# Optimization experiments

Measured on AMD Instinct MI355X. Metric: run time of the kernel, lower is better.

The kernel has to match this reference:

```python
import jax, jax.numpy as jnp
import numpy as np

N_NODES = 50000
N_EDGES = 800000
NUM_GRAPHS = 256
H = 128          # h_dim
C = H + 1        # CGConv channels = 129
Z = 2 * C + 1    # concat(x_i, x_j, edge_attr) = 259
N_GRAPH_LAYERS = 5
N_FC = 3
OUT_DIM = 1


def setup_inputs() -> dict:
    key = jax.random.key(0)
    ks = jax.random.split(key, 12)
    atoms = jax.random.randint(ks[0], (N_NODES,), 0, 119)
    pos = jax.random.normal(ks[1], (N_NODES, 3), dtype=jnp.float32)
    edge_index = jax.random.randint(ks[2], (2, N_EDGES), 0, N_NODES)
    batch = jnp.sort(jax.random.randint(ks[3], (N_NODES,), 0, NUM_GRAPHS))
    s = 0.05
    emb = jax.random.normal(ks[4], (119, H), dtype=jnp.float32)
    Wf = jax.random.normal(ks[5], (N_GRAPH_LAYERS, Z, C), dtype=jnp.float32) * s
    bf = jnp.zeros((N_GRAPH_LAYERS, C), dtype=jnp.float32)
    Ws = jax.random.normal(ks[6], (N_GRAPH_LAYERS, Z, C), dtype=jnp.float32) * s
    bs = jnp.zeros((N_GRAPH_LAYERS, C), dtype=jnp.float32)
    Wfc = jax.random.normal(ks[7], (N_FC, C, C), dtype=jnp.float32) * s
    bfc = jnp.zeros((N_FC, C), dtype=jnp.float32)
    Wout = jax.random.normal(ks[8], (C, OUT_DIM), dtype=jnp.float32) * s
    bout = jnp.zeros((OUT_DIM,), dtype=jnp.float32)
    return {"atoms": atoms, "pos": pos, "edge_index": edge_index, "batch": batch,
            "emb": emb, "Wf": Wf, "bf": bf, "Ws": Ws, "bs": bs,
            "Wfc": Wfc, "bfc": bfc, "Wout": Wout, "bout": bout}


def reference(atoms, pos, edge_index, batch, emb, Wf, bf, Ws, bs, Wfc, bfc, Wout, bout):
    n = atoms.shape[0]
    src, dst = edge_index[0], edge_index[1]  # PyG: x_j = x[src], x_i = x[dst], aggregate at dst
    # edge_attr = ||pos[src] - pos[dst]||, shape [E, 1]
    edge_attr = jnp.linalg.norm(pos[src] - pos[dst], axis=-1, keepdims=True)
    # node features: atom embedding + z-coordinate -> [N, 129]
    x = jnp.concatenate([emb[atoms], pos[:, 2:3]], axis=-1)
    for l in range(Wf.shape[0]):
        z = jnp.concatenate([x[dst], x[src], edge_attr], axis=-1)  # [E, 259]
        m = jax.nn.sigmoid(z @ Wf[l] + bf[l]) * jax.nn.softplus(z @ Ws[l] + bs[l])
        x = x + jax.ops.segment_sum(m, dst, num_segments=n)  # CGConv: aggr='add' + residual
    # mean pooling per graph
    sums = jax.ops.segment_sum(x, batch, num_segments=NUM_GRAPHS)
    cnts = jax.ops.segment_sum(jnp.ones((n, 1), x.dtype), batch, num_segments=NUM_GRAPHS)
    g = sums / jnp.maximum(cnts, 1.0)
    for l in range(Wfc.shape[0]):
        g = g @ Wfc[l] + bfc[l]
    return g @ Wout + bout
```

## Files before the change

kernel.cpp:

```cpp
#include <hip/hip_runtime.h>
#include <math.h>

#define N_NODES 50000
#define N_EDGES 800000
#define NUM_GRAPHS 256
#define NPADROWS 50048
#define CAP 64
#define XS 132
#define SCLN -1.44269504088896f
#define SCLP 1.44269504088896f
#define C693 0.69314718056f

typedef __attribute__((ext_vector_type(8))) short short8;
typedef __attribute__((ext_vector_type(4))) float f32x4;
typedef __attribute__((ext_vector_type(2))) float f32x2;

__device__ __forceinline__ float fast_rcp(float x) {
#if __has_builtin(__builtin_amdgcn_rcpf)
  return __builtin_amdgcn_rcpf(x);
#else
  return 1.0f / x;
#endif
}
__device__ __forceinline__ float EX2(float x) {
#if __has_builtin(__builtin_amdgcn_exp2f)
  return __builtin_amdgcn_exp2f(x);
#else
  return exp2f(x);
#endif
}
__device__ __forceinline__ float LG2(float x) {
#if __has_builtin(__builtin_amdgcn_logf)
  return __builtin_amdgcn_logf(x);
#else
  return log2f(x);
#endif
}
__device__ __forceinline__ unsigned f2bf(float x) {
  unsigned u = __float_as_uint(x);
  return (u + 0x7fffu + ((u >> 16) & 1u)) >> 16;
}
__device__ __forceinline__ float u2f(unsigned u) { return __uint_as_float(u); }
__device__ __forceinline__ f32x2 mk2(float a, float b) {
  f32x2 r; r.x = a; r.y = b; return r;
}
__device__ __forceinline__ f32x2 unp(unsigned u) {
  return mk2(u2f(u << 16), u2f(u & 0xffff0000u));
}
__device__ __forceinline__ void edge_ch2(f32x2 gf, f32x2 gs, float cmul, f32x2& acc) {
  f32x2 den = mk2(EX2(gf.x), EX2(gf.y)) + 1.0f;
  f32x2 lg = mk2(LG2(1.0f + EX2(-fabsf(gs.x))), LG2(1.0f + EX2(-fabsf(gs.y))));
  f32x2 sp = lg + __builtin_elementwise_max(gs, (f32x2)0.0f);
  f32x2 rt = mk2(fast_rcp(den.x), fast_rcp(den.y)) * sp;
  acc = __builtin_elementwise_fma(rt, (f32x2)cmul, acc);
}

__global__ void init_x(const int* __restrict__ atoms, const float* __restrict__ pos,
                       const float* __restrict__ emb, float* __restrict__ xf,
                       unsigned* __restrict__ xbu, float4* __restrict__ pos4) {
  int n = blockIdx.x;
  int t = threadIdx.x;
  int a = atoms[n];
  float2 e = *(const float2*)(emb + (size_t)a * 128 + 2 * t);
  xf[(size_t)n * XS + 2 * t] = e.x;
  xf[(size_t)n * XS + 2 * t + 1] = e.y;
  xbu[(size_t)n * 64 + t] = f2bf(e.x) | (f2bf(e.y) << 16);
  if (t == 0) xf[(size_t)n * XS + 128] = pos[n * 3 + 2];
  if (t == 1) pos4[n] = make_float4(pos[3 * n], pos[3 * n + 1], pos[3 * n + 2], 0.f);
}

__global__ void prep_b(const float* __restrict__ Wf, const float* __restrict__ Ws,
                       uint4* __restrict__ Bp, float* __restrict__ W128) {
  int idx = blockIdx.x * 256 + threadIdx.x;
  if (idx < 5 * 4 * 9 * 4 * 64) {
    int lane = idx & 63;
    int t = idx >> 6;
    int ks = t & 3; t >>= 2;
    int ct = t % 9; t /= 9;
    int g = t & 3;
    int l = t >> 2;
    const float* W = (g >= 2) ? Ws : Wf;
    int col = ct * 16 + (lane & 15);
    int kb = ks * 32 + (lane >> 4) * 8;
    unsigned u[4];
#pragma unroll
    for (int p = 0; p < 4; ++p) {
      unsigned lo = 0, hi = 0;
      if (col < 129) {
        int k0 = kb + 2 * p, k1 = k0 + 1;
        int r0 = (g & 1) ? 129 + k0 : k0;
        int r1 = (g & 1) ? 129 + k1 : k1;
        lo = f2bf(W[(size_t)(l * 259 + r0) * 129 + col]);
        hi = f2bf(W[(size_t)(l * 259 + r1) * 129 + col]);
      }
      u[p] = lo | (hi << 16);
    }
    Bp[idx] = make_uint4(u[0], u[1], u[2], u[3]);
  } else {
    int j = idx - 5 * 4 * 9 * 4 * 64;
    if (j >= 5 * 4 * 129) return;
    int c = j % 129;
    int t = j / 129;
    int g = t & 3;
    int l = t >> 2;
    const float* W = (g >= 2) ? Ws : Wf;
    int row = (g & 1) ? 257 : 128;
    W128[(l * 4 + g) * 129 + c] = W[(size_t)(l * 259 + row) * 129 + c];
  }
}

__global__ void build_csr(const int* __restrict__ ei, const float4* __restrict__ pos4,
                          int* __restrict__ cnt, int2* __restrict__ csr) {
  int e = blockIdx.x * 256 + threadIdx.x;
  if (e >= N_EDGES) return;
  int s = ei[e];
  int d = ei[N_EDGES + e];
  float4 ps = pos4[s];
  float4 pd = pos4[d];
  float dx = ps.x - pd.x, dy = ps.y - pd.y, dz = ps.z - pd.z;
  float ea = sqrtf(dx * dx + dy * dy + dz * dz);
  int p = atomicAdd(&cnt[d], 1);
  if (p < CAP) csr[d * CAP + p] = make_int2(s, __float_as_int(ea));
}

__global__ void offsets_k(const int* __restrict__ batch, int* __restrict__ goff) {
  int n = blockIdx.x * 256 + threadIdx.x;
  if (n > N_NODES) return;
  int b = (n < N_NODES) ? batch[n] : NUM_GRAPHS;
  int bp = (n > 0) ? batch[n - 1] : -1;
  for (int g = bp + 1; g <= b; ++g) goff[g] = n;
}

__global__ __launch_bounds__(256) void gemm_mfma(
    const unsigned* __restrict__ xbu, const float* __restrict__ xf,
    const uint4* __restrict__ Bp, const float* __restrict__ W128,
    const float* __restrict__ bfL, const float* __restrict__ bsL,
    unsigned short* __restrict__ Pdh, unsigned short* __restrict__ Pfs,
    unsigned* __restrict__ Pd128c, unsigned* __restrict__ Pc128, int layer) {
  __shared__ short smA[32 * 136];
  int n0 = blockIdx.x * 32;
  int tid = threadIdx.x;
  for (int ch = tid; ch < 512; ch += 256) {
    int row = ch >> 4, cq = ch & 15;
    *(uint4*)(&smA[row * 136 + cq * 8]) =
        *(const uint4*)(xbu + (size_t)(n0 + row) * 64 + cq * 4);
  }
  __syncthreads();
  int g = tid >> 6;
  int l = tid & 63;
  int q = l >> 4, c16 = l & 15;
  const short8* Bp8 = (const short8*)Bp;
  int bbase = (layer * 4 + g) * 9 * 4;
  f32x4 acc[2][9];
#pragma unroll
  for (int rt = 0; rt < 2; ++rt)
#pragma unroll
    for (int ct = 0; ct < 9; ++ct) acc[rt][ct] = (f32x4){0.f, 0.f, 0.f, 0.f};
#pragma unroll
  for (int ks = 0; ks < 4; ++ks) {
    short8 a0 = *(const short8*)(&smA[c16 * 136 + (ks * 4 + q) * 8]);
    short8 a1 = *(const short8*)(&smA[(16 + c16) * 136 + (ks * 4 + q) * 8]);
#pragma unroll
    for (int ct = 0; ct < 9; ++ct) {
      short8 b = Bp8[(size_t)(bbase + ct * 4 + ks) * 64 + l];
      acc[0][ct] = __builtin_amdgcn_mfma_f32_16x16x32_bf16(a0, b, acc[0][ct], 0, 0, 0);
      acc[1][ct] = __builtin_amdgcn_mfma_f32_16x16x32_bf16(a1, b, acc[1][ct], 0, 0, 0);
    }
  }
  const float* W1g = W128 + (layer * 4 + g) * 129;
  float x128[2][4];
#pragma unroll
  for (int rt = 0; rt < 2; ++rt)
#pragma unroll
    for (int r = 0; r < 4; ++r)
      x128[rt][r] = xf[(size_t)(n0 + rt * 16 + q * 4 + r) * XS + 128];
  float scale = (g < 2) ? SCLN : SCLP;
  unsigned short* dstp = (g & 1) ? Pfs : Pdh;
  int soff = (g >= 2) ? 2 : 0;
  unsigned short* c128p = (g & 1) ? (unsigned short*)Pc128 : (unsigned short*)Pd128c;
  int c128o = (g >= 2) ? 1 : 0;
#pragma unroll
  for (int ct = 0; ct < 9; ++ct) {
    int col = ct * 16 + c16;
    float w1 = (col <= 128) ? W1g[col] : 0.0f;
    float bias = 0.0f;
    if (g == 0 && col <= 128) bias = bfL[col];
    if (g == 2 && col <= 128) bias = bsL[col];
#pragma unroll
    for (int rt = 0; rt < 2; ++rt) {
#pragma unroll
      for (int r = 0; r < 4; ++r) {
        int row = n0 + rt * 16 + q * 4 + r;
        float v = scale * (acc[rt][ct][r] + x128[rt][r] * w1 + bias);
        unsigned short bv = (unsigned short)f2bf(v);
        if (col < 128) {
          dstp[(size_t)row * 256 + ((col >> 1) << 2) + soff + (col & 1)] = bv;
        } else if (col == 128) {
          c128p[2 * (size_t)row + c128o] = bv;
        }
      }
    }
  }
}

__global__ __launch_bounds__(256) void edge_agg(
    const unsigned short* __restrict__ Pdh, const unsigned short* __restrict__ Pfs,
    const unsigned* __restrict__ Pd128c, const unsigned* __restrict__ Pc128,
    float* __restrict__ xf, unsigned* __restrict__ xbu, const int* __restrict__ cnt,
    const int2* __restrict__ csr, const float* __restrict__ WfL,
    const float* __restrict__ WsL) {
  int lane = threadIdx.x & 63;
  int half = lane >> 5;
  int l5 = lane & 31;
  int n = blockIdx.x * 4 + (threadIdx.x >> 6);
  if (n >= N_NODES) return;
  int nu = __builtin_amdgcn_readfirstlane(n);
  const float* wfl = WfL + 258 * 129;
  const float* wsl = WsL + 258 * 129;
  uint4 pdv = *(const uint4*)(Pdh + (size_t)nu * 256 + 8 * l5);
  f32x2 bfa = unp(pdv.x), bsa = unp(pdv.y), bfb = unp(pdv.z), bsb = unp(pdv.w);
  float2 wfa0 = *(const float2*)(wfl + 4 * l5);
  float2 wfb0 = *(const float2*)(wfl + 4 * l5 + 2);
  float2 wsa0 = *(const float2*)(wsl + 4 * l5);
  float2 wsb0 = *(const float2*)(wsl + 4 * l5 + 2);
  f32x2 wfa = mk2(SCLN * wfa0.x, SCLN * wfa0.y), wfb = mk2(SCLN * wfb0.x, SCLN * wfb0.y);
  f32x2 wsa = mk2(SCLP * wsa0.x, SCLP * wsa0.y), wsb = mk2(SCLP * wsb0.x, SCLP * wsb0.y);
  unsigned pd1 = Pd128c[nu];
  float bfc8 = u2f(pd1 << 16), bsc8 = u2f(pd1 & 0xffff0000u);
  float wfc8 = SCLN * wfl[128], wsc8 = SCLP * wsl[128];
  int m = cnt[nu];
  if (m > CAP) m = CAP;
  const int4* cb4 = (const int4*)(csr + (size_t)nu * CAP);
  float maskC = half ? 0.0f : C693;
  f32x2 accA = (f32x2)0.0f, accB = (f32x2)0.0f;

#define DO_PAIR(qq, CM)                                                        \
  {                                                                            \
    int s_ = half ? qq.z : qq.x;                                               \
    f32x2 ea_ = (f32x2)__int_as_float(half ? qq.w : qq.y);                     \
    uint4 g_ = *(const uint4*)(Pfs + (size_t)s_ * 256 + 8 * l5);               \
    edge_ch2(__builtin_elementwise_fma(ea_, wfa, bfa + unp(g_.x)),             \
             __builtin_elementwise_fma(ea_, wsa, bsa + unp(g_.y)), CM, accA);  \
    edge_ch2(__builtin_elementwise_fma(ea_, wfb, bfb + unp(g_.z)),             \
             __builtin_elementwise_fma(ea_, wsb, bsb + unp(g_.w)), CM, accB);  \
  }

  int Pf = m >> 1;
  int p = 0;
  for (; p + 1 < Pf; p += 2) {
    int4 q0 = cb4[p];
    int4 q1 = cb4[p + 1];
    DO_PAIR(q0, C693);
    DO_PAIR(q1, C693);
  }
  if (p < Pf) {
    int4 q0 = cb4[p];
    DO_PAIR(q0, C693);
  }
  if (m & 1) {
    int4 q = cb4[Pf];
    int s_ = q.x;
    f32x2 ea_ = (f32x2)__int_as_float(q.y);
    uint4 g_ = *(const uint4*)(Pfs + (size_t)s_ * 256 + 8 * l5);
    edge_ch2(__builtin_elementwise_fma(ea_, wfa, bfa + unp(g_.x)),
             __builtin_elementwise_fma(ea_, wsa, bsa + unp(g_.y)), maskC, accA);
    edge_ch2(__builtin_elementwise_fma(ea_, wfb, bfb + unp(g_.z)),
             __builtin_elementwise_fma(ea_, wsb, bsb + unp(g_.w)), maskC, accB);
  }
#undef DO_PAIR

  accA.x += __shfl_xor(accA.x, 32, 64);
  accA.y += __shfl_xor(accA.y, 32, 64);
  accB.x += __shfl_xor(accB.x, 32, 64);
  accB.y += __shfl_xor(accB.y, 32, 64);

  float v2 = 0.f;
  if (lane < m) {
    int2 se = csr[(size_t)nu * CAP + lane];
    float ea = __int_as_float(se.y);
    unsigned pc = Pc128[se.x];
    float f2 = u2f(pc << 16), s2 = u2f(pc & 0xffff0000u);
    float gf2 = fmaf(ea, wfc8, bfc8 + f2);
    float gs2 = fmaf(ea, wsc8, bsc8 + s2);
    float sp2 = LG2(1.0f + EX2(-fabsf(gs2))) + fmaxf(gs2, 0.0f);
    v2 = C693 * fast_rcp(1.0f + EX2(gf2)) * sp2;
  }
#pragma unroll
  for (int off = 32; off; off >>= 1) v2 += __shfl_down(v2, off, 64);

  size_t xo = (size_t)nu * XS;
  if (half == 0) {
    float4 xv = *(const float4*)(xf + xo + 4 * l5);
    float4 res = make_float4(xv.x + accA.x, xv.y + accA.y, xv.z + accB.x, xv.w + accB.y);
    *(float4*)(xf + xo + 4 * l5) = res;
    *(uint2*)(xbu + (size_t)nu * 64 + 2 * l5) =
        make_uint2(f2bf(res.x) | (f2bf(res.y) << 16), f2bf(res.z) | (f2bf(res.w) << 16));
  }
  if (lane == 0) xf[xo + 128] += v2;
}

__global__ void pool2(const float* __restrict__ xf, const int* __restrict__ goff,
                      float* __restrict__ gsum) {
  int gph = blockIdx.x >> 2;
  int q = blockIdx.x & 3;
  int t = threadIdx.x;
  if (t >= 129) return;
  int s = goff[gph], e = goff[gph + 1];
  int len = e - s;
  int chunk = (len + 3) >> 2;
  int a = s + q * chunk;
  int b = a + chunk; if (b > e) b = e;
  if (a >= b) return;
  float acc = 0.f;
  for (int n = a; n < b; ++n) acc += xf[(size_t)n * XS + t];
  atomicAdd(&gsum[gph * XS + t], acc);
}

__global__ void fcout(const float* __restrict__ gsum, const int* __restrict__ goff,
                      const float* __restrict__ Wfc, const float* __restrict__ bfc,
                      const float* __restrict__ Wout, const float* __restrict__ bout,
                      float* __restrict__ out) {
  __shared__ float buf[2][132];
  __shared__ float red[3];
  int i = blockIdx.x;
  int t = threadIdx.x;
  int len = goff[i + 1] - goff[i];
  float inv = fast_rcp(fmaxf((float)len, 1.0f));
  if (t < 129) buf[0][t] = gsum[i * XS + t] * inv;
  __syncthreads();
  int cur = 0;
#pragma unroll
  for (int l = 0; l < 3; ++l) {
    float s = 0.f;
    if (t < 129) {
      s = bfc[l * 129 + t];
      const float* W = Wfc + (size_t)l * 129 * 129;
#pragma unroll 4
      for (int k = 0; k < 129; ++k) s += buf[cur][k] * W[k * 129 + t];
    }
    __syncthreads();
    if (t < 129) buf[1 - cur][t] = s;
    cur = 1 - cur;
    __syncthreads();
  }
  float p = (t < 129) ? buf[cur][t] * Wout[t] : 0.f;
#pragma unroll
  for (int off = 32; off; off >>= 1) p += __shfl_down(p, off, 64);
  if ((t & 63) == 0) red[t >> 6] = p;
  __syncthreads();
  if (t == 0) out[i] = red[0] + red[1] + red[2] + bout[0];
}

extern "C" void kernel_launch(void* const* d_in, const int* in_sizes, int n_in,
                              void* d_out, int out_size, void* d_ws, size_t ws_size,
                              hipStream_t stream) {
  const int* atoms = (const int*)d_in[0];
  const float* pos = (const float*)d_in[1];
  const int* ei = (const int*)d_in[2];
  const int* batch = (const int*)d_in[3];
  const float* emb = (const float*)d_in[4];
  const float* Wf = (const float*)d_in[5];
  const float* bfp = (const float*)d_in[6];
  const float* Ws = (const float*)d_in[7];
  const float* bsp = (const float*)d_in[8];
  const float* Wfc = (const float*)d_in[9];
  const float* bfc = (const float*)d_in[10];
  const float* Wout = (const float*)d_in[11];
  const float* bout = (const float*)d_in[12];
  float* outp = (float*)d_out;

  uint4* Bp = (uint4*)d_ws;
  float* xf = (float*)(Bp + 46080);
  unsigned* xbu = (unsigned*)(xf + (size_t)NPADROWS * XS);
  unsigned short* Pdh = (unsigned short*)(xbu + (size_t)NPADROWS * 64);
  unsigned short* Pfs = Pdh + (size_t)NPADROWS * 256;
  float4* pos4 = (float4*)(Pfs + (size_t)NPADROWS * 256);
  float* W128 = (float*)(pos4 + N_NODES);
  float* gsum = W128 + 2580;
  int* goff = (int*)(gsum + 256 * XS);
  int* cnt = goff + 260;
  int2* csr = (int2*)(cnt + N_NODES);
  unsigned* Pd128c = (unsigned*)(csr + (size_t)N_NODES * CAP);
  unsigned* Pc128 = Pd128c + NPADROWS;

  hipMemsetAsync(cnt, 0, N_NODES * sizeof(int), stream);
  hipMemsetAsync(gsum, 0, 256 * XS * sizeof(float), stream);

  init_x<<<N_NODES, 64, 0, stream>>>(atoms, pos, emb, xf, xbu, pos4);
  prep_b<<<(5 * 4 * 9 * 4 * 64 + 5 * 4 * 129 + 255) / 256, 256, 0, stream>>>(Wf, Ws, Bp,
                                                                             W128);
  build_csr<<<(N_EDGES + 255) / 256, 256, 0, stream>>>(ei, pos4, cnt, csr);
  offsets_k<<<(N_NODES + 256) / 256, 256, 0, stream>>>(batch, goff);

  for (int l = 0; l < 5; ++l) {
    gemm_mfma<<<NPADROWS / 32, 256, 0, stream>>>(xbu, xf, Bp, W128, bfp + l * 129,
                                                 bsp + l * 129, Pdh, Pfs, Pd128c,
                                                 Pc128, l);
    edge_agg<<<(N_NODES + 3) / 4, 256, 0, stream>>>(Pdh, Pfs, Pd128c, Pc128, xf, xbu,
                                                    cnt, csr,
                                                    Wf + (size_t)l * 259 * 129,
                                                    Ws + (size_t)l * 259 * 129);
  }

  pool2<<<NUM_GRAPHS * 4, 192, 0, stream>>>(xf, goff, gsum);
  fcout<<<NUM_GRAPHS, 192, 0, stream>>>(gsum, goff, Wfc, bfc, Wout, bout, outp);
}
```

Baseline: 757.6 us.

## Stage GEMM outputs in LDS for coalesced stores; software-pipeline edge gathers

The GEMM epilogue now writes its bf16 results into shared-memory tiles and then copies them to the global Pdh/Pfs arrays with 16-byte coalesced stores, replacing the scattered 2-byte global writes. In edge_agg, the unrolled two-pair loop becomes a software-pipelined loop that prefetches the next CSR entry and its source-row gather while the current one is computed. This costs extra LDS (about 34 KB per block), which may reduce occupancy, plus one more block barrier. The prefetch also keeps more registers live.

```diff
diff --git a/kernel.cpp b/kernel.cpp
--- a/kernel.cpp
+++ b/kernel.cpp
@@ -10,6 +10,7 @@
 #define SCLN -1.44269504088896f
 #define SCLP 1.44269504088896f
 #define C693 0.69314718056f
+#define LROW 264
 
 typedef __attribute__((ext_vector_type(8))) short short8;
 typedef __attribute__((ext_vector_type(4))) float f32x4;
@@ -138,6 +139,8 @@
     unsigned short* __restrict__ Pdh, unsigned short* __restrict__ Pfs,
     unsigned* __restrict__ Pd128c, unsigned* __restrict__ Pc128, int layer) {
   __shared__ short smA[32 * 136];
+  __shared__ unsigned short ldsD[32 * LROW];
+  __shared__ unsigned short ldsS[32 * LROW];
   int n0 = blockIdx.x * 32;
   int tid = threadIdx.x;
   for (int ch = tid; ch < 512; ch += 256) {
@@ -175,7 +178,7 @@
     for (int r = 0; r < 4; ++r)
       x128[rt][r] = xf[(size_t)(n0 + rt * 16 + q * 4 + r) * XS + 128];
   float scale = (g < 2) ? SCLN : SCLP;
-  unsigned short* dstp = (g & 1) ? Pfs : Pdh;
+  unsigned short* ldsO = (g & 1) ? ldsS : ldsD;
   int soff = (g >= 2) ? 2 : 0;
   unsigned short* c128p = (g & 1) ? (unsigned short*)Pc128 : (unsigned short*)Pd128c;
   int c128o = (g >= 2) ? 1 : 0;
@@ -190,16 +193,26 @@
     for (int rt = 0; rt < 2; ++rt) {
 #pragma unroll
       for (int r = 0; r < 4; ++r) {
-        int row = n0 + rt * 16 + q * 4 + r;
+        int rl = rt * 16 + q * 4 + r;
         float v = scale * (acc[rt][ct][r] + x128[rt][r] * w1 + bias);
         unsigned short bv = (unsigned short)f2bf(v);
         if (col < 128) {
-          dstp[(size_t)row * 256 + ((col >> 1) << 2) + soff + (col & 1)] = bv;
+          ldsO[rl * LROW + ((col >> 1) << 2) + soff + (col & 1)] = bv;
         } else if (col == 128) {
-          c128p[2 * (size_t)row + c128o] = bv;
+          c128p[2 * (size_t)(n0 + rl) + c128o] = bv;
         }
       }
     }
+  }
+  __syncthreads();
+#pragma unroll
+  for (int i = tid; i < 2048; i += 256) {
+    int img = i >> 10;
+    int c = i & 1023;
+    int row = c >> 5, part = c & 31;
+    const unsigned short* src = (img ? ldsS : ldsD) + row * LROW + part * 8;
+    unsigned short* dst = (img ? Pfs : Pdh) + (size_t)(n0 + row) * 256 + part * 8;
+    *(uint4*)dst = *(const uint4*)src;
   }
 }
 
@@ -231,43 +244,49 @@
   int m = cnt[nu];
   if (m > CAP) m = CAP;
   const int4* cb4 = (const int4*)(csr + (size_t)nu * CAP);
+  const uint4* Pfq = (const uint4*)Pfs;
   float maskC = half ? 0.0f : C693;
   f32x2 accA = (f32x2)0.0f, accB = (f32x2)0.0f;
 
-#define DO_PAIR(qq, CM)                                                        \
+#define GATHER(qq) Pfq[(size_t)(half ? qq.z : qq.x) * 32 + l5]
+#define COMPUTE(qq, gg, CM)                                                    \
   {                                                                            \
-    int s_ = half ? qq.z : qq.x;                                               \
     f32x2 ea_ = (f32x2)__int_as_float(half ? qq.w : qq.y);                     \
-    uint4 g_ = *(const uint4*)(Pfs + (size_t)s_ * 256 + 8 * l5);               \
-    edge_ch2(__builtin_elementwise_fma(ea_, wfa, bfa + unp(g_.x)),             \
-             __builtin_elementwise_fma(ea_, wsa, bsa + unp(g_.y)), CM, accA);  \
-    edge_ch2(__builtin_elementwise_fma(ea_, wfb, bfb + unp(g_.z)),             \
-             __builtin_elementwise_fma(ea_, wsb, bsb + unp(g_.w)), CM, accB);  \
+    edge_ch2(__builtin_elementwise_fma(ea_, wfa, bfa + unp(gg.x)),             \
+             __builtin_elementwise_fma(ea_, wsa, bsa + unp(gg.y)), CM, accA);  \
+    edge_ch2(__builtin_elementwise_fma(ea_, wfb, bfb + unp(gg.z)),             \
+             __builtin_elementwise_fma(ea_, wsb, bsb + unp(gg.w)), CM, accB);  \
   }
 
   int Pf = m >> 1;
-  int p = 0;
-  for (; p + 1 < Pf; p += 2) {
-    int4 q0 = cb4[p];
-    int4 q1 = cb4[p + 1];
-    DO_PAIR(q0, C693);
-    DO_PAIR(q1, C693);
-  }
-  if (p < Pf) {
-    int4 q0 = cb4[p];
-    DO_PAIR(q0, C693);
+  int4 qc = make_int4(0, 0, 0, 0);
+  uint4 gc = make_uint4(0, 0, 0, 0);
+  if (Pf > 0) {
+    qc = cb4[0];
+    gc = GATHER(qc);
+  }
+  for (int p = 0; p < Pf; ++p) {
+    int4 qn = qc;
+    uint4 gn = gc;
+    if (p + 1 < Pf) {
+      qn = cb4[p + 1];
+      gn = GATHER(qn);
+    }
+    COMPUTE(qc, gc, C693);
+    qc = qn;
+    gc = gn;
   }
   if (m & 1) {
-    int4 q = cb4[Pf];
-    int s_ = q.x;
-    f32x2 ea_ = (f32x2)__int_as_float(q.y);
-    uint4 g_ = *(const uint4*)(Pfs + (size_t)s_ * 256 + 8 * l5);
-    edge_ch2(__builtin_elementwise_fma(ea_, wfa, bfa + unp(g_.x)),
-             __builtin_elementwise_fma(ea_, wsa, bsa + unp(g_.y)), maskC, accA);
-    edge_ch2(__builtin_elementwise_fma(ea_, wfb, bfb + unp(g_.z)),
-             __builtin_elementwise_fma(ea_, wsb, bsb + unp(g_.w)), maskC, accB);
-  }
-#undef DO_PAIR
+    int4 qt = cb4[Pf];
+    f32x2 ea_ = (f32x2)__int_as_float(qt.y);
+    uint4 gt = Pfq[(size_t)qt.x * 32 + l5];
+    edge_ch2(__builtin_elementwise_fma(ea_, wfa, bfa + unp(gt.x)),
+             __builtin_elementwise_fma(ea_, wsa, bsa + unp(gt.y)), maskC, accA);
+    edge_ch2(__builtin_elementwise_fma(ea_, wfb, bfb + unp(gt.z)),
+             __builtin_elementwise_fma(ea_, wsb, bsb + unp(gt.w)), maskC, accB);
+  }
+#undef GATHER
+#undef COMPUTE
 
   accA.x += __shfl_xor(accA.x, 32, 64);
   accA.y += __shfl_xor(accA.y, 32, 64);
```

Result: faster. 738.6 us (-2.5%).
